# Kernel optimization log

Hardware: AMD Instinct MI355X
Metric: run time of the kernel (lower is better)

Reference implementation:

```python
import jax, jax.numpy as jnp
import numpy as np

N_NODES = 100000
N_EDGES = 1600000
IN_DIM = 128
HEADS = 4
OUT_DIM = 32
NEG_SLOPE = 0.2  # PyG GATConv default negative_slope


def setup_inputs() -> dict:
    key = jax.random.key(0)
    k_x, k_e, k_w, k_as, k_ad = jax.random.split(key, 5)
    x = jax.random.normal(k_x, (N_NODES, IN_DIM), dtype=jnp.float32)
    edge_index = jax.random.randint(k_e, (2, N_EDGES), 0, N_NODES, dtype=jnp.int64)
    # Glorot-style init for learned parameters (GATConv lin + attention vectors)
    W = jax.random.normal(k_w, (IN_DIM, HEADS * OUT_DIM), dtype=jnp.float32) / np.sqrt(IN_DIM)
    att_src = jax.random.normal(k_as, (HEADS, OUT_DIM), dtype=jnp.float32) / np.sqrt(OUT_DIM)
    att_dst = jax.random.normal(k_ad, (HEADS, OUT_DIM), dtype=jnp.float32) / np.sqrt(OUT_DIM)
    bias = jnp.zeros((HEADS * OUT_DIM,), dtype=jnp.float32)
    return {"x": x, "edge_index": edge_index, "W": W, "att_src": att_src,
            "att_dst": att_dst, "bias": bias}


def reference(x, edge_index, W, att_src, att_dst, bias):
    N = x.shape[0]
    H, D = att_src.shape
    # PyG GATConv default: add self loops
    loop = jnp.arange(N, dtype=edge_index.dtype)
    src = jnp.concatenate([edge_index[0], loop])  # message sources  [E+N]
    dst = jnp.concatenate([edge_index[1], loop])  # message targets  [E+N]

    h = (x @ W).reshape(N, H, D)                          # [N, H, D]
    a_src = jnp.einsum('nhd,hd->nh', h, att_src)          # [N, H]
    a_dst = jnp.einsum('nhd,hd->nh', h, att_dst)          # [N, H]

    # per-edge attention logits, LeakyReLU(neg_slope=0.2)
    e = jax.nn.leaky_relu(a_src[src] + a_dst[dst], NEG_SLOPE)  # [E+N, H]

    # segment softmax over edges grouped by target node (numerically stable)
    e_max = jax.ops.segment_max(e, dst, num_segments=N)        # [N, H]
    e_max = jnp.where(jnp.isfinite(e_max), e_max, jnp.float32(0))
    ex = jnp.exp(e - e_max[dst])                               # [E+N, H]
    denom = jax.ops.segment_sum(ex, dst, num_segments=N)       # [N, H]
    alpha = ex / (denom[dst] + jnp.float32(1e-16))             # [E+N, H]

    # weighted scatter-aggregate of source features
    msg = h[src] * alpha[:, :, None]                           # [E+N, H, D]
    out = jax.ops.segment_sum(msg, dst, num_segments=N)        # [N, H, D]
    out = out.reshape(N, H * D) + bias                         # concat heads + bias
    return jax.nn.elu(out)                                     # wrapper ELU
```

## Files before the change

kernel.cpp:

```cpp
#include <hip/hip_runtime.h>
#include <hip/hip_fp16.h>
#include <math.h>

#define N_NODES 100000
#define N_EDGES 1600000
#define IN_DIM 128
#define F_DIM 128
#define NEG_SLOPE 0.2f

#define BUCKW_LOG 7
#define NBUCK 784
#define NBLK 128
#define EPB 12500
#define G_TOT (NBUCK * NBLK)
#define SC_CHUNK 4096
#define SC_NB ((G_TOT + SC_CHUNK - 1) / SC_CHUNK)
#define CSR_CAP (N_EDGES + NBUCK * 384)

typedef short v8s __attribute__((ext_vector_type(8)));
typedef float v4f __attribute__((ext_vector_type(4)));

static __device__ __forceinline__ unsigned short f2bf(float f) {
    unsigned u = __float_as_uint(f);
    u += 0x7fffu + ((u >> 16) & 1u);
    return (unsigned short)(u >> 16);
}
static __device__ __forceinline__ float bf2f(unsigned s) { return __uint_as_float(s << 16); }
static __device__ __forceinline__ float lo2f(unsigned u) { return __uint_as_float(u << 16); }
static __device__ __forceinline__ float hi2f(unsigned u) { return __uint_as_float(u & 0xffff0000u); }

__global__ __launch_bounds__(256) void k_wprep(const float* __restrict__ W,
                                               unsigned short* __restrict__ Wt) {
    int i = blockIdx.x * 256 + threadIdx.x;
    int n = i >> 7, k = i & 127;
    Wt[n * 128 + k] = f2bf(W[k * 128 + n]);
}

__global__ __launch_bounds__(256) void k_gemm(const float* __restrict__ x,
                                              const unsigned short* __restrict__ Wt,
                                              unsigned short* __restrict__ h16,
                                              const float* __restrict__ att_src,
                                              const float* __restrict__ att_dst,
                                              float* __restrict__ a_src,
                                              float* __restrict__ a_dst) {
    __shared__ unsigned short As[64][136];
    __shared__ unsigned short Bs[128][136];
    __shared__ float attl[256];
    const int t  = threadIdx.x;
    const int n0 = blockIdx.x * 64;

    attl[t] = (t < 128) ? att_src[t] : att_dst[t - 128];

    {
        int row = t >> 2, k0 = (t & 3) * 32;
        int n = n0 + row;
        #pragma unroll
        for (int i = 0; i < 4; i++) {
            float4 va = make_float4(0.f,0.f,0.f,0.f), vb = va;
            if (n < N_NODES) {
                const float* p = x + (size_t)n * IN_DIM + k0 + i * 8;
                va = *(const float4*)p;
                vb = *(const float4*)(p + 4);
            }
            uint4 u;
            u.x = f2bf(va.x) | ((unsigned)f2bf(va.y) << 16);
            u.y = f2bf(va.z) | ((unsigned)f2bf(va.w) << 16);
            u.z = f2bf(vb.x) | ((unsigned)f2bf(vb.y) << 16);
            u.w = f2bf(vb.z) | ((unsigned)f2bf(vb.w) << 16);
            *(uint4*)&As[row][k0 + i * 8] = u;
        }
    }
    {
        int nr = t >> 1, s0 = (t & 1) * 64;
        const uint4* src = (const uint4*)(Wt + nr * 128 + s0);
        #pragma unroll
        for (int i = 0; i < 8; i++)
            *(uint4*)&Bs[nr][s0 + i * 8] = src[i];
    }
    __syncthreads();

    const int w = t >> 6, lane = t & 63;
    const int mr = lane & 15, quad = lane >> 4;
    const int m0 = w * 16;

    v4f acc[8];
    #pragma unroll
    for (int nt = 0; nt < 8; nt++) acc[nt] = (v4f){0.f, 0.f, 0.f, 0.f};

    #pragma unroll
    for (int kk = 0; kk < 4; kk++) {
        int kof = kk * 32 + quad * 8;
        v8s a = *(const v8s*)&As[m0 + mr][kof];
        #pragma unroll
        for (int nt = 0; nt < 8; nt++) {
            v8s b = *(const v8s*)&Bs[nt * 16 + mr][kof];
            acc[nt] = __builtin_amdgcn_mfma_f32_16x16x32_bf16(a, b, acc[nt], 0, 0, 0);
        }
    }

    #pragma unroll
    for (int nt = 0; nt < 8; nt++)
        #pragma unroll
        for (int r = 0; r < 4; r++)
            As[m0 + quad * 4 + r][nt * 16 + mr] = f2bf(acc[nt][r]);
    __syncthreads();
    {
        int row = m0 + (lane >> 2);
        int c0  = (lane & 3) * 32;
        int n = n0 + row;
        if (n < N_NODES) {
            float ds = 0.f, dd = 0.f;
            #pragma unroll
            for (int i = 0; i < 4; i++) {
                uint4 v = *(const uint4*)&As[row][c0 + i * 8];
                *(uint4*)&h16[(size_t)n * F_DIM + c0 + i * 8] = v;
                float f0 = lo2f(v.x), f1 = hi2f(v.x);
                float f2 = lo2f(v.y), f3 = hi2f(v.y);
                float f4 = lo2f(v.z), f5 = hi2f(v.z);
                float f6 = lo2f(v.w), f7 = hi2f(v.w);
                const float* ps = &attl[c0 + i * 8];
                const float* pd = &attl[128 + c0 + i * 8];
                ds += f0*ps[0] + f1*ps[1] + f2*ps[2] + f3*ps[3]
                    + f4*ps[4] + f5*ps[5] + f6*ps[6] + f7*ps[7];
                dd += f0*pd[0] + f1*pd[1] + f2*pd[2] + f3*pd[3]
                    + f4*pd[4] + f5*pd[5] + f6*pd[6] + f7*pd[7];
            }
            int hd = lane & 3;
            a_src[n * 4 + hd] = ds;
            a_dst[n * 4 + hd] = dd;
        }
    }
}

__global__ __launch_bounds__(256) void k_bhist(const int* __restrict__ ei_dst,
                                               int* __restrict__ G) {
    __shared__ int hist[NBUCK];
    for (int i = threadIdx.x; i < NBUCK; i += 256) hist[i] = 0;
    __syncthreads();
    int e0 = blockIdx.x * EPB;
    for (int i = threadIdx.x; i < EPB; i += 256) {
        int d = ei_dst[e0 + i];
        atomicAdd(&hist[d >> BUCKW_LOG], 1);
    }
    __syncthreads();
    for (int b = threadIdx.x; b < NBUCK; b += 256)
        G[b * NBLK + blockIdx.x] = hist[b];
}

__global__ __launch_bounds__(256) void k_scanp(const int* __restrict__ a,
                                               int* __restrict__ part) {
    int base = blockIdx.x * SC_CHUNK + threadIdx.x * 16;
    int s = 0;
    #pragma unroll
    for (int i = 0; i < 16; i++) {
        int idx = base + i;
        if (idx < G_TOT) s += a[idx];
    }
    __shared__ int wsum[4];
    for (int off = 32; off >= 1; off >>= 1) s += __shfl_down(s, off, 64);
    if ((threadIdx.x & 63) == 0) wsum[threadIdx.x >> 6] = s;
    __syncthreads();
    if (threadIdx.x == 0) part[blockIdx.x] = wsum[0] + wsum[1] + wsum[2] + wsum[3];
}

__global__ void k_scant(int* part, int* boff) {
    int lane = threadIdx.x & 63;
    int v = (lane < SC_NB) ? part[lane] : 0;
    int x = v;
    #pragma unroll
    for (int off = 1; off < 64; off <<= 1) {
        int y = __shfl_up(x, off, 64);
        if (lane >= off) x += y;
    }
    if (lane < SC_NB) part[lane] = x - v;
    if (lane == 0) boff[NBUCK] = N_EDGES;
}

__global__ __launch_bounds__(256) void k_scand(int* __restrict__ a,
                                               const int* __restrict__ part,
                                               int* __restrict__ boff) {
    __shared__ int tsum[256];
    int tid  = threadIdx.x;
    int base = blockIdx.x * SC_CHUNK + tid * 16;
    int v[16]; int s = 0;
    #pragma unroll
    for (int i = 0; i < 16; i++) {
        int idx = base + i;
        v[i] = (idx < G_TOT) ? a[idx] : 0;
        s += v[i];
    }
    tsum[tid] = s;
    __syncthreads();
    for (int off = 1; off < 256; off <<= 1) {
        int y = (tid >= off) ? tsum[tid - off] : 0;
        __syncthreads();
        tsum[tid] += y;
        __syncthreads();
    }
    int run = part[blockIdx.x] + tsum[tid] - s;
    #pragma unroll
    for (int i = 0; i < 16; i++) {
        int idx = base + i;
        if (idx < G_TOT) {
            a[idx] = run;
            if (idx % NBLK == 0) boff[idx / NBLK] = run;
        }
        run += v[i];
    }
}

__global__ __launch_bounds__(256) void k_bscat(const int* __restrict__ ei,
                                               const int* __restrict__ G,
                                               int* __restrict__ ebuf) {
    __shared__ int base[NBUCK];
    for (int b = threadIdx.x; b < NBUCK; b += 256)
        base[b] = G[b * NBLK + blockIdx.x];
    __syncthreads();
    int e0 = blockIdx.x * EPB;
    for (int i = threadIdx.x; i < EPB; i += 256) {
        int s = ei[e0 + i];
        int d = ei[N_EDGES + e0 + i];
        int b = d >> BUCKW_LOG;
        int pos = atomicAdd(&base[b], 1);
        ebuf[pos] = s | ((d & 127) << 17);
    }
}

__global__ __launch_bounds__(256) void k_csrfin(const int* __restrict__ ebuf,
                                                const int* __restrict__ boff,
                                                const float* __restrict__ a_src,
                                                const float* __restrict__ a_dst,
                                                int2* __restrict__ ebounds,
                                                int* __restrict__ csr2,
                                                __half* __restrict__ pbuf) {
    __shared__ int cnt[128];
    __shared__ int off[128];
    int b = blockIdx.x;
    int beg = boff[b], end = boff[b + 1];
    int padded_base = beg + b * 384;
    if (threadIdx.x < 128) cnt[threadIdx.x] = 0;
    __syncthreads();
    for (int j = beg + threadIdx.x; j < end; j += 256)
        atomicAdd(&cnt[(ebuf[j] >> 17) & 127], 1);
    __syncthreads();
    if (threadIdx.x == 0) {
        int run = padded_base;
        for (int i = 0; i < 128; i++) { off[i] = run; run += (cnt[i] + 3) & ~3; }
    }
    __syncthreads();
    if (threadIdx.x < 128) {
        int node = (b << BUCKW_LOG) + threadIdx.x;
        int c = cnt[threadIdx.x];
        if (node < N_NODES) {
            ebounds[node] = make_int2(off[threadIdx.x], off[threadIdx.x] + c);
            int cpad = (c + 3) & ~3;
            for (int k = c; k < cpad; k++) {
                int pos = off[threadIdx.x] + k;
                csr2[pos] = node;
                *(uint2*)&pbuf[(size_t)pos * 4] = make_uint2(0u, 0u);
            }
        }
        cnt[threadIdx.x] = 0;
    }
    __syncthreads();
    for (int j = beg + threadIdx.x; j < end; j += 256) {
        int p = ebuf[j];
        int dl = (p >> 17) & 127;
        int s = p & 0x1ffff;
        int r = atomicAdd(&cnt[dl], 1);
        int pos = off[dl] + r;
        csr2[pos] = s;
        int d = (b << BUCKW_LOG) + dl;
        float4 as = *(const float4*)&a_src[s * 4];
        float4 ad = *(const float4*)&a_dst[d * 4];
        float e0 = as.x + ad.x; e0 = e0 > 0.f ? e0 : NEG_SLOPE * e0;
        float e1 = as.y + ad.y; e1 = e1 > 0.f ? e1 : NEG_SLOPE * e1;
        float e2 = as.z + ad.z; e2 = e2 > 0.f ? e2 : NEG_SLOPE * e2;
        float e3 = as.w + ad.w; e3 = e3 > 0.f ? e3 : NEG_SLOPE * e3;
        __half2 lo = __floats2half2_rn(__expf(e0), __expf(e1));
        __half2 hi = __floats2half2_rn(__expf(e2), __expf(e3));
        *(uint2*)&pbuf[(size_t)pos * 4] =
            make_uint2(*(unsigned*)&lo, *(unsigned*)&hi);
    }
}

__global__ __launch_bounds__(256) void k_agg(const uint4* __restrict__ h16x4,
                                             const float* __restrict__ a_src,
                                             const float* __restrict__ a_dst,
                                             const int2* __restrict__ ebounds,
                                             const int* __restrict__ csr2,
                                             const __half* __restrict__ pbuf,
                                             const float* __restrict__ bias,
                                             float* __restrict__ out) {
    int n = (blockIdx.x * 256 + threadIdx.x) >> 6;
    if (n >= N_NODES) return;
    int lane = threadIdx.x & 63;
    int grp = lane >> 4, g = lane & 15, hd = g >> 2;

    float p0 = 0.f;
    if (grp == 0) {
        float e0 = a_src[n * 4 + hd] + a_dst[n * 4 + hd];
        e0 = e0 > 0.f ? e0 : NEG_SLOPE * e0;
        p0 = __expf(e0);
    }
    uint4 hs = h16x4[(size_t)n * 16 + g];
    float l  = p0;
    float a0 = p0 * lo2f(hs.x), a1 = p0 * hi2f(hs.x);
    float a2 = p0 * lo2f(hs.y), a3 = p0 * hi2f(hs.y);
    float a4 = p0 * lo2f(hs.z), a5 = p0 * hi2f(hs.z);
    float a6 = p0 * lo2f(hs.w), a7 = p0 * hi2f(hs.w);

    int2 eb = ebounds[n];
    int beg = eb.x, cnt = eb.y - eb.x;
    const int* sp = csr2 + beg + grp;
    const __half* pp = pbuf + (size_t)(beg + grp) * 4 + hd;
    int steps = (cnt + 3) >> 2;
    int t = 0;
    for (; t + 2 <= steps; t += 2) {
        int s0 = sp[4 * t];
        int s1 = sp[4 * t + 4];
        float q0 = __half2float(pp[16 * t]);
        float q1 = __half2float(pp[16 * t + 16]);
        uint4 h0 = h16x4[(size_t)s0 * 16 + g];
        uint4 h1 = h16x4[(size_t)s1 * 16 + g];
        l  += q0 + q1;
        a0 += q0 * lo2f(h0.x) + q1 * lo2f(h1.x);
        a1 += q0 * hi2f(h0.x) + q1 * hi2f(h1.x);
        a2 += q0 * lo2f(h0.y) + q1 * lo2f(h1.y);
        a3 += q0 * hi2f(h0.y) + q1 * hi2f(h1.y);
        a4 += q0 * lo2f(h0.z) + q1 * lo2f(h1.z);
        a5 += q0 * hi2f(h0.z) + q1 * hi2f(h1.z);
        a6 += q0 * lo2f(h0.w) + q1 * lo2f(h1.w);
        a7 += q0 * hi2f(h0.w) + q1 * hi2f(h1.w);
    }
    if (t < steps) {
        int s0 = sp[4 * t];
        float q0 = __half2float(pp[16 * t]);
        uint4 h0 = h16x4[(size_t)s0 * 16 + g];
        l  += q0;
        a0 += q0 * lo2f(h0.x);
        a1 += q0 * hi2f(h0.x);
        a2 += q0 * lo2f(h0.y);
        a3 += q0 * hi2f(h0.y);
        a4 += q0 * lo2f(h0.z);
        a5 += q0 * hi2f(h0.z);
        a6 += q0 * lo2f(h0.w);
        a7 += q0 * hi2f(h0.w);
    }
    #define RED2(v) v += __shfl_xor(v, 16, 64); v += __shfl_xor(v, 32, 64);
    RED2(l); RED2(a0); RED2(a1); RED2(a2); RED2(a3);
    RED2(a4); RED2(a5); RED2(a6); RED2(a7);
    #undef RED2

    if (grp == 0) {
        float inv = 1.f / (l + 1e-16f);
        float4 b0 = *(const float4*)&bias[g * 8];
        float4 b1 = *(const float4*)&bias[g * 8 + 4];
        float o0 = a0 * inv + b0.x, o1 = a1 * inv + b0.y;
        float o2 = a2 * inv + b0.z, o3 = a3 * inv + b0.w;
        float o4 = a4 * inv + b1.x, o5 = a5 * inv + b1.y;
        float o6 = a6 * inv + b1.z, o7 = a7 * inv + b1.w;
        o0 = o0 > 0.f ? o0 : __expf(o0) - 1.f;
        o1 = o1 > 0.f ? o1 : __expf(o1) - 1.f;
        o2 = o2 > 0.f ? o2 : __expf(o2) - 1.f;
        o3 = o3 > 0.f ? o3 : __expf(o3) - 1.f;
        o4 = o4 > 0.f ? o4 : __expf(o4) - 1.f;
        o5 = o5 > 0.f ? o5 : __expf(o5) - 1.f;
        o6 = o6 > 0.f ? o6 : __expf(o6) - 1.f;
        o7 = o7 > 0.f ? o7 : __expf(o7) - 1.f;
        *(float4*)&out[(size_t)n * F_DIM + g * 8]     = make_float4(o0, o1, o2, o3);
        *(float4*)&out[(size_t)n * F_DIM + g * 8 + 4] = make_float4(o4, o5, o6, o7);
    }
}

extern "C" void kernel_launch(void* const* d_in, const int* in_sizes, int n_in,
                              void* d_out, int out_size, void* d_ws, size_t ws_size,
                              hipStream_t stream) {
    const float* x       = (const float*)d_in[0];
    const int*   ei      = (const int*)d_in[1];
    const float* W       = (const float*)d_in[2];
    const float* att_src = (const float*)d_in[3];
    const float* att_dst = (const float*)d_in[4];
    const float* bias    = (const float*)d_in[5];
    float*       out     = (float*)d_out;

    char* ws = (char*)d_ws;
    unsigned short* h16 = (unsigned short*)ws; ws += (size_t)N_NODES * F_DIM * 2;
    unsigned short* Wt  = (unsigned short*)ws; ws += (size_t)IN_DIM * F_DIM * 2;
    float* a_src  = (float*)ws; ws += (size_t)N_NODES * 4 * 4;
    float* a_dst  = (float*)ws; ws += (size_t)N_NODES * 4 * 4;
    int*   G      = (int*)ws;   ws += (size_t)G_TOT * 4;
    int*   part   = (int*)ws;   ws += 1024;
    int*   boff   = (int*)ws;   ws += 4096;
    int2*  ebounds= (int2*)ws;  ws += (size_t)N_NODES * 8 + 512;
    int*   ebuf   = (int*)ws;   ws += (size_t)N_EDGES * 4;
    int*   csr2   = (int*)ws;   ws += (size_t)CSR_CAP * 4;
    __half* pbuf  = (__half*)ws; ws += (size_t)CSR_CAP * 4 * 2;

    k_wprep<<<64, 256, 0, stream>>>(W, Wt);
    k_gemm<<<(N_NODES + 63) / 64, 256, 0, stream>>>(x, Wt, h16, att_src, att_dst, a_src, a_dst);

    k_bhist<<<NBLK, 256, 0, stream>>>(ei + N_EDGES, G);
    k_scanp<<<SC_NB, 256, 0, stream>>>(G, part);
    k_scant<<<1, 64, 0, stream>>>(part, boff);
    k_scand<<<SC_NB, 256, 0, stream>>>(G, part, boff);
    k_bscat<<<NBLK, 256, 0, stream>>>(ei, G, ebuf);
    k_csrfin<<<NBUCK, 256, 0, stream>>>(ebuf, boff, a_src, a_dst, ebounds, csr2, pbuf);

    k_agg<<<(N_NODES * 64 + 255) / 256, 256, 0, stream>>>((const uint4*)h16, a_src, a_dst, ebounds, csr2, pbuf, bias, out);
}
```

Measured before the change: 301.0 us.

## Replace bucketed two-pass CSR build with per-node degree histogram and atomic scatter

Replaces the bucket histogram, bucket scatter and per-bucket finalisation with a per-node degree count, a padded exclusive scan that writes ebounds and cursors directly, and a single scatter kernel that uses global atomics on per-node cursors to place edges and their exp logits. The degree histogram runs as extra blocks in the GEMM kernel, and the separate W transpose kernel is folded into the GEMM's shared-memory load. This drops several launches and the intermediate ebuf pass, at the cost of many contended global atomics and a nondeterministic edge order within each node.

```diff
diff --git a/kernel.cpp b/kernel.cpp
--- a/kernel.cpp
+++ b/kernel.cpp
@@ -3,19 +3,21 @@
 #include <math.h>
 
 #define N_NODES 100000
+#define N_PAD   100352
 #define N_EDGES 1600000
 #define IN_DIM 128
 #define F_DIM 128
 #define NEG_SLOPE 0.2f
 
-#define BUCKW_LOG 7
-#define NBUCK 784
-#define NBLK 128
-#define EPB 12500
-#define G_TOT (NBUCK * NBLK)
+#define GB 1563
+#define HB 200
+#define EPH 8000
+#define SB 200
+#define EPS 8000
+
 #define SC_CHUNK 4096
-#define SC_NB ((G_TOT + SC_CHUNK - 1) / SC_CHUNK)
-#define CSR_CAP (N_EDGES + NBUCK * 384)
+#define SC_NB ((N_PAD + SC_CHUNK - 1) / SC_CHUNK)
+#define CSR_CAP (N_EDGES + 3 * N_PAD + 64)
 
 typedef short v8s __attribute__((ext_vector_type(8)));
 typedef float v4f __attribute__((ext_vector_type(4)));
@@ -25,24 +27,31 @@
     u += 0x7fffu + ((u >> 16) & 1u);
     return (unsigned short)(u >> 16);
 }
-static __device__ __forceinline__ float bf2f(unsigned s) { return __uint_as_float(s << 16); }
 static __device__ __forceinline__ float lo2f(unsigned u) { return __uint_as_float(u << 16); }
 static __device__ __forceinline__ float hi2f(unsigned u) { return __uint_as_float(u & 0xffff0000u); }
 
-__global__ __launch_bounds__(256) void k_wprep(const float* __restrict__ W,
-                                               unsigned short* __restrict__ Wt) {
-    int i = blockIdx.x * 256 + threadIdx.x;
-    int n = i >> 7, k = i & 127;
-    Wt[n * 128 + k] = f2bf(W[k * 128 + n]);
-}
-
-__global__ __launch_bounds__(256) void k_gemm(const float* __restrict__ x,
-                                              const unsigned short* __restrict__ Wt,
+__global__ __launch_bounds__(256) void k_main(const float* __restrict__ x,
+                                              const float* __restrict__ W,
+                                              const int* __restrict__ ei_dst,
                                               unsigned short* __restrict__ h16,
                                               const float* __restrict__ att_src,
                                               const float* __restrict__ att_dst,
                                               float* __restrict__ a_src,
-                                              float* __restrict__ a_dst) {
+                                              float* __restrict__ a_dst,
+                                              int* __restrict__ deg) {
+    if (blockIdx.x >= GB) {
+        int hb = blockIdx.x - GB;
+        const int4* p = (const int4*)(ei_dst + hb * EPH);
+        for (int i = threadIdx.x; i < EPH / 4; i += 256) {
+            int4 d = p[i];
+            atomicAdd(&deg[d.x], 1);
+            atomicAdd(&deg[d.y], 1);
+            atomicAdd(&deg[d.z], 1);
+            atomicAdd(&deg[d.w], 1);
+        }
+        return;
+    }
+
     __shared__ unsigned short As[64][136];
     __shared__ unsigned short Bs[128][136];
     __shared__ float attl[256];
@@ -71,11 +80,12 @@
         }
     }
     {
-        int nr = t >> 1, s0 = (t & 1) * 64;
-        const uint4* src = (const uint4*)(Wt + nr * 128 + s0);
         #pragma unroll
-        for (int i = 0; i < 8; i++)
-            *(uint4*)&Bs[nr][s0 + i * 8] = src[i];
+        for (int i = 0; i < 64; i++) {
+            int j = (i << 8) + t;
+            int k = j >> 7, n = j & 127;
+            Bs[n][k] = f2bf(W[j]);
+        }
     }
     __syncthreads();
 
@@ -132,29 +142,14 @@
     }
 }
 
-__global__ __launch_bounds__(256) void k_bhist(const int* __restrict__ ei_dst,
-                                               int* __restrict__ G) {
-    __shared__ int hist[NBUCK];
-    for (int i = threadIdx.x; i < NBUCK; i += 256) hist[i] = 0;
-    __syncthreads();
-    int e0 = blockIdx.x * EPB;
-    for (int i = threadIdx.x; i < EPB; i += 256) {
-        int d = ei_dst[e0 + i];
-        atomicAdd(&hist[d >> BUCKW_LOG], 1);
-    }
-    __syncthreads();
-    for (int b = threadIdx.x; b < NBUCK; b += 256)
-        G[b * NBLK + blockIdx.x] = hist[b];
-}
-
-__global__ __launch_bounds__(256) void k_scanp(const int* __restrict__ a,
+__global__ __launch_bounds__(256) void k_scanp(const int* __restrict__ deg,
                                                int* __restrict__ part) {
     int base = blockIdx.x * SC_CHUNK + threadIdx.x * 16;
     int s = 0;
     #pragma unroll
     for (int i = 0; i < 16; i++) {
         int idx = base + i;
-        if (idx < G_TOT) s += a[idx];
+        if (idx < N_PAD) s += (deg[idx] + 3) & ~3;
     }
     __shared__ int wsum[4];
     for (int off = 32; off >= 1; off >>= 1) s += __shfl_down(s, off, 64);
@@ -163,7 +158,7 @@
     if (threadIdx.x == 0) part[blockIdx.x] = wsum[0] + wsum[1] + wsum[2] + wsum[3];
 }
 
-__global__ void k_scant(int* part, int* boff) {
+__global__ void k_scant(int* part) {
     int lane = threadIdx.x & 63;
     int v = (lane < SC_NB) ? part[lane] : 0;
     int x = v;
@@ -173,21 +168,23 @@
         if (lane >= off) x += y;
     }
     if (lane < SC_NB) part[lane] = x - v;
-    if (lane == 0) boff[NBUCK] = N_EDGES;
-}
-
-__global__ __launch_bounds__(256) void k_scand(int* __restrict__ a,
+}
+
+__global__ __launch_bounds__(256) void k_scand(const int* __restrict__ deg,
                                                const int* __restrict__ part,
-                                               int* __restrict__ boff) {
+                                               int2* __restrict__ ebounds,
+                                               int* __restrict__ cursor,
+                                               int* __restrict__ csr2,
+                                               __half* __restrict__ pbuf) {
     __shared__ int tsum[256];
     int tid  = threadIdx.x;
     int base = blockIdx.x * SC_CHUNK + tid * 16;
-    int v[16]; int s = 0;
+    int c[16]; int s = 0;
     #pragma unroll
     for (int i = 0; i < 16; i++) {
         int idx = base + i;
-        v[i] = (idx < G_TOT) ? a[idx] : 0;
-        s += v[i];
+        c[i] = (idx < N_PAD) ? deg[idx] : 0;
+        s += (c[i] + 3) & ~3;
     }
     tsum[tid] = s;
     __syncthreads();
@@ -201,87 +198,51 @@
     #pragma unroll
     for (int i = 0; i < 16; i++) {
         int idx = base + i;
-        if (idx < G_TOT) {
-            a[idx] = run;
-            if (idx % NBLK == 0) boff[idx / NBLK] = run;
-        }
-        run += v[i];
-    }
-}
-
-__global__ __launch_bounds__(256) void k_bscat(const int* __restrict__ ei,
-                                               const int* __restrict__ G,
-                                               int* __restrict__ ebuf) {
-    __shared__ int base[NBUCK];
-    for (int b = threadIdx.x; b < NBUCK; b += 256)
-        base[b] = G[b * NBLK + blockIdx.x];
-    __syncthreads();
-    int e0 = blockIdx.x * EPB;
-    for (int i = threadIdx.x; i < EPB; i += 256) {
-        int s = ei[e0 + i];
-        int d = ei[N_EDGES + e0 + i];
-        int b = d >> BUCKW_LOG;
-        int pos = atomicAdd(&base[b], 1);
-        ebuf[pos] = s | ((d & 127) << 17);
-    }
-}
-
-__global__ __launch_bounds__(256) void k_csrfin(const int* __restrict__ ebuf,
-                                                const int* __restrict__ boff,
-                                                const float* __restrict__ a_src,
-                                                const float* __restrict__ a_dst,
-                                                int2* __restrict__ ebounds,
-                                                int* __restrict__ csr2,
-                                                __half* __restrict__ pbuf) {
-    __shared__ int cnt[128];
-    __shared__ int off[128];
-    int b = blockIdx.x;
-    int beg = boff[b], end = boff[b + 1];
-    int padded_base = beg + b * 384;
-    if (threadIdx.x < 128) cnt[threadIdx.x] = 0;
-    __syncthreads();
-    for (int j = beg + threadIdx.x; j < end; j += 256)
-        atomicAdd(&cnt[(ebuf[j] >> 17) & 127], 1);
-    __syncthreads();
-    if (threadIdx.x == 0) {
-        int run = padded_base;
-        for (int i = 0; i < 128; i++) { off[i] = run; run += (cnt[i] + 3) & ~3; }
-    }
-    __syncthreads();
-    if (threadIdx.x < 128) {
-        int node = (b << BUCKW_LOG) + threadIdx.x;
-        int c = cnt[threadIdx.x];
-        if (node < N_NODES) {
-            ebounds[node] = make_int2(off[threadIdx.x], off[threadIdx.x] + c);
-            int cpad = (c + 3) & ~3;
-            for (int k = c; k < cpad; k++) {
-                int pos = off[threadIdx.x] + k;
-                csr2[pos] = node;
+        if (idx < N_PAD) {
+            int cc = c[i], cp = (cc + 3) & ~3;
+            ebounds[idx] = make_int2(run, run + cc);
+            cursor[idx]  = run;
+            for (int k = cc; k < cp; k++) {
+                int pos = run + k;
+                csr2[pos] = idx;
                 *(uint2*)&pbuf[(size_t)pos * 4] = make_uint2(0u, 0u);
             }
-        }
-        cnt[threadIdx.x] = 0;
-    }
-    __syncthreads();
-    for (int j = beg + threadIdx.x; j < end; j += 256) {
-        int p = ebuf[j];
-        int dl = (p >> 17) & 127;
-        int s = p & 0x1ffff;
-        int r = atomicAdd(&cnt[dl], 1);
-        int pos = off[dl] + r;
-        csr2[pos] = s;
-        int d = (b << BUCKW_LOG) + dl;
-        float4 as = *(const float4*)&a_src[s * 4];
-        float4 ad = *(const float4*)&a_dst[d * 4];
-        float e0 = as.x + ad.x; e0 = e0 > 0.f ? e0 : NEG_SLOPE * e0;
-        float e1 = as.y + ad.y; e1 = e1 > 0.f ? e1 : NEG_SLOPE * e1;
-        float e2 = as.z + ad.z; e2 = e2 > 0.f ? e2 : NEG_SLOPE * e2;
-        float e3 = as.w + ad.w; e3 = e3 > 0.f ? e3 : NEG_SLOPE * e3;
-        __half2 lo = __floats2half2_rn(__expf(e0), __expf(e1));
-        __half2 hi = __floats2half2_rn(__expf(e2), __expf(e3));
-        *(uint2*)&pbuf[(size_t)pos * 4] =
-            make_uint2(*(unsigned*)&lo, *(unsigned*)&hi);
-    }
+            run += cp;
+        }
+    }
+}
+
+__global__ __launch_bounds__(1024) void k_scat(const int* __restrict__ ei,
+                                               int* __restrict__ cursor,
+                                               const float* __restrict__ a_src,
+                                               const float* __restrict__ a_dst,
+                                               int* __restrict__ csr2,
+                                               __half* __restrict__ pbuf) {
+    const int4* ps = (const int4*)(ei + blockIdx.x * EPS);
+    const int4* pd = (const int4*)(ei + N_EDGES + blockIdx.x * EPS);
+    #define PLACE(sv, dv) {                                                    \
+        int pos = atomicAdd(&cursor[dv], 1);                                   \
+        csr2[pos] = (sv);                                                      \
+        float4 as = *(const float4*)&a_src[(sv) * 4];                          \
+        float4 ad = *(const float4*)&a_dst[(dv) * 4];                          \
+        float e0 = as.x + ad.x; e0 = e0 > 0.f ? e0 : NEG_SLOPE * e0;           \
+        float e1 = as.y + ad.y; e1 = e1 > 0.f ? e1 : NEG_SLOPE * e1;           \
+        float e2 = as.z + ad.z; e2 = e2 > 0.f ? e2 : NEG_SLOPE * e2;           \
+        float e3 = as.w + ad.w; e3 = e3 > 0.f ? e3 : NEG_SLOPE * e3;           \
+        __half2 lo = __floats2half2_rn(__expf(e0), __expf(e1));                \
+        __half2 hi = __floats2half2_rn(__expf(e2), __expf(e3));                \
+        *(uint2*)&pbuf[(size_t)pos * 4] =                                      \
+            make_uint2(*(unsigned*)&lo, *(unsigned*)&hi);                      \
+    }
+    for (int i = threadIdx.x; i < EPS / 4; i += 1024) {
+        int4 s4 = ps[i];
+        int4 d4 = pd[i];
+        PLACE(s4.x, d4.x);
+        PLACE(s4.y, d4.y);
+        PLACE(s4.z, d4.z);
+        PLACE(s4.w, d4.w);
+    }
+    #undef PLACE
 }
 
 __global__ __launch_bounds__(256) void k_agg(const uint4* __restrict__ h16x4,
@@ -386,26 +347,21 @@
 
     char* ws = (char*)d_ws;
     unsigned short* h16 = (unsigned short*)ws; ws += (size_t)N_NODES * F_DIM * 2;
-    unsigned short* Wt  = (unsigned short*)ws; ws += (size_t)IN_DIM * F_DIM * 2;
-    float* a_src  = (float*)ws; ws += (size_t)N_NODES * 4 * 4;
-    float* a_dst  = (float*)ws; ws += (size_t)N_NODES * 4 * 4;
-    int*   G      = (int*)ws;   ws += (size_t)G_TOT * 4;
+    float* a_src  = (float*)ws; ws += (size_t)N_PAD * 16;
+    float* a_dst  = (float*)ws; ws += (size_t)N_PAD * 16;
+    int*   deg    = (int*)ws;   ws += (size_t)N_PAD * 4;
+    int*   cursor = (int*)ws;   ws += (size_t)N_PAD * 4;
+    int2*  ebounds= (int2*)ws;  ws += (size_t)N_PAD * 8;
     int*   part   = (int*)ws;   ws += 1024;
-    int*   boff   = (int*)ws;   ws += 4096;
-    int2*  ebounds= (int2*)ws;  ws += (size_t)N_NODES * 8 + 512;
-    int*   ebuf   = (int*)ws;   ws += (size_t)N_EDGES * 4;
     int*   csr2   = (int*)ws;   ws += (size_t)CSR_CAP * 4;
-    __half* pbuf  = (__half*)ws; ws += (size_t)CSR_CAP * 4 * 2;
-
-    k_wprep<<<64, 256, 0, stream>>>(W, Wt);
-    k_gemm<<<(N_NODES + 63) / 64, 256, 0, stream>>>(x, Wt, h16, att_src, att_dst, a_src, a_dst);
-
-    k_bhist<<<NBLK, 256, 0, stream>>>(ei + N_EDGES, G);
-    k_scanp<<<SC_NB, 256, 0, stream>>>(G, part);
-    k_scant<<<1, 64, 0, stream>>>(part, boff);
-    k_scand<<<SC_NB, 256, 0, stream>>>(G, part, boff);
-    k_bscat<<<NBLK, 256, 0, stream>>>(ei, G, ebuf);
-    k_csrfin<<<NBUCK, 256, 0, stream>>>(ebuf, boff, a_src, a_dst, ebounds, csr2, pbuf);
-
+    __half* pbuf  = (__half*)ws; ws += (size_t)CSR_CAP * 8;
+
+    hipMemsetAsync(deg, 0, (size_t)N_PAD * 4, stream);
+    k_main<<<GB + HB, 256, 0, stream>>>(x, W, ei + N_EDGES, h16, att_src, att_dst,
+                                        a_src, a_dst, deg);
+    k_scanp<<<SC_NB, 256, 0, stream>>>(deg, part);
+    k_scant<<<1, 64, 0, stream>>>(part);
+    k_scand<<<SC_NB, 256, 0, stream>>>(deg, part, ebounds, cursor, csr2, pbuf);
+    k_scat<<<SB, 1024, 0, stream>>>(ei, cursor, a_src, a_dst, csr2, pbuf);
     k_agg<<<(N_NODES * 64 + 255) / 256, 256, 0, stream>>>((const uint4*)h16, a_src, a_dst, ebounds, csr2, pbuf, bias, out);
 }
```

After: 394.6 us. +31.1%, slower.
